# Kernel tuning notes

Measured on AMD Instinct MI355X. Metric: run time of the kernel, lower is better.

## Reference

```python
import jax, jax.numpy as jnp
import numpy as np

DIM, HEADS, RANK = 768, 12, 64
HEAD_DIM = DIM // HEADS

def _xavier(key, shape):
    fan_in, fan_out = shape[1], shape[0]
    std = (2.0 / (fan_in + fan_out)) ** 0.5
    return std * jax.random.normal(key, shape, dtype=jnp.float32)

def setup_inputs() -> dict:
    key = jax.random.key(0)
    ks = jax.random.split(key, 12)
    B, N = 8, 1024
    x = jax.random.normal(ks[0], (B, N, DIM), dtype=jnp.float32)
    params = {}
    for i, nm in enumerate(['Q', 'K', 'V']):
        params[f'W_{nm}0'] = _xavier(ks[1 + 3 * i], (DIM, RANK))
        params[f'W_{nm}1'] = _xavier(ks[2 + 3 * i], (HEADS, RANK))
        params[f'W_{nm}2'] = _xavier(ks[3 + 3 * i], (HEAD_DIM, RANK))
    proj_w = _xavier(ks[10], (DIM, DIM))
    proj_b = jnp.zeros((DIM,), dtype=jnp.float32)
    return dict(x=x, W_Q0=params['W_Q0'], W_Q1=params['W_Q1'], W_Q2=params['W_Q2'],
                W_K0=params['W_K0'], W_K1=params['W_K1'], W_K2=params['W_K2'],
                W_V0=params['W_V0'], W_V1=params['W_V1'], W_V2=params['W_V2'],
                proj_w=proj_w, proj_b=proj_b)

def _cp_proj(xh, W2, W1, W0, B, N, H, hd):
    # xh: [B,N,H,hd]; contract head_dim with W2 and heads with W1 -> [B,N,R], then expand to dim via W0
    t = jnp.einsum('blnd,dr,nr->blr', xh, W2, W1)
    out = jnp.einsum('blr,mr->blm', t, W0)          # [B,N,dim]
    return out.reshape(B, N, H, hd).transpose(0, 2, 1, 3)  # [B,H,N,hd]

def reference(x, W_Q0, W_Q1, W_Q2, W_K0, W_K1, W_K2, W_V0, W_V1, W_V2, proj_w, proj_b):
    B, N, C = x.shape
    H = W_Q1.shape[0]
    hd = C // H
    scale = hd ** -0.5
    xh = x.reshape(B, N, H, hd)
    q = _cp_proj(xh, W_Q2, W_Q1, W_Q0, B, N, H, hd)
    k = _cp_proj(xh, W_K2, W_K1, W_K0, B, N, H, hd)
    v = _cp_proj(xh, W_V2, W_V1, W_V0, B, N, H, hd)
    attn = jax.nn.softmax(jnp.einsum('bhqd,bhkd->bhqk', q, k) * scale, axis=-1)
    out = jnp.einsum('bhqk,bhkd->bhqd', attn, v).transpose(0, 2, 1, 3).reshape(B, N, C)
    return out @ proj_w.T + proj_b
```

## Files before the change

### kernel.cpp

```cpp
#include <hip/hip_runtime.h>

typedef unsigned short u16;
typedef __attribute__((ext_vector_type(8))) short bf16x8;
typedef __attribute__((ext_vector_type(4))) float f32x4;
typedef __attribute__((ext_vector_type(4))) unsigned short u16x4;
typedef __attribute__((ext_vector_type(8))) unsigned short u16x8;

#define AS1 __attribute__((address_space(1)))
#define AS3 __attribute__((address_space(3)))

__device__ __forceinline__ u16 f2b(float f) {
    unsigned u = __float_as_uint(f);
    unsigned r = 0x7fffu + ((u >> 16) & 1u);
    return (u16)((u + r) >> 16);
}

__device__ __forceinline__ unsigned packtrunc(float p0, float p1) {
#if __has_builtin(__builtin_amdgcn_perm)
    return __builtin_amdgcn_perm(__float_as_uint(p1), __float_as_uint(p0), 0x07060302u);
#else
    return (__float_as_uint(p0) >> 16) | (__float_as_uint(p1) & 0xffff0000u);
#endif
}

#if __has_builtin(__builtin_amdgcn_exp2f)
#define EXP2(x) __builtin_amdgcn_exp2f(x)
#else
#define EXP2(x) exp2f(x)
#endif

__device__ unsigned g_cnt[2];
__device__ unsigned g_gen[2];

__device__ __forceinline__ void gbar(int i, unsigned nblk) {
    __syncthreads();
    if (threadIdx.x == 0) {
        __threadfence();
        const unsigned my = __hip_atomic_load(&g_gen[i], __ATOMIC_RELAXED,
                                              __HIP_MEMORY_SCOPE_AGENT);
        const unsigned v = __hip_atomic_fetch_add(&g_cnt[i], 1u, __ATOMIC_ACQ_REL,
                                                  __HIP_MEMORY_SCOPE_AGENT);
        if (v == nblk - 1u) {
            __hip_atomic_store(&g_cnt[i], 0u, __ATOMIC_RELAXED,
                               __HIP_MEMORY_SCOPE_AGENT);
            __threadfence();
            __hip_atomic_fetch_add(&g_gen[i], 1u, __ATOMIC_ACQ_REL,
                                   __HIP_MEMORY_SCOPE_AGENT);
        } else {
            unsigned spins = 0;
            while (__hip_atomic_load(&g_gen[i], __ATOMIC_ACQUIRE,
                                     __HIP_MEMORY_SCOPE_AGENT) == my) {
                __builtin_amdgcn_s_sleep(2);
                if (++spins > (1u << 22)) break;
            }
        }
        __threadfence();
    }
    __syncthreads();
}

__device__ __forceinline__ void phaseA(
    const int bid, const int t, char* smem,
    const float* __restrict__ X,
    const float* __restrict__ Wq0, const float* __restrict__ Wq1, const float* __restrict__ Wq2,
    const float* __restrict__ Wk0, const float* __restrict__ Wk1, const float* __restrict__ Wk2,
    const float* __restrict__ Wv0, const float* __restrict__ Wv1, const float* __restrict__ Wv2,
    const float* __restrict__ PW,
    u16* __restrict__ T, u16* __restrict__ tvt,
    u16* __restrict__ MqkT, u16* __restrict__ Dcat)
{
    const f32x4 zero4 = {0.f, 0.f, 0.f, 0.f};
    if (bid < 384) {
        u16*   As  = (u16*)smem;
        u16*   Bs  = (u16*)(smem + 8192);
        float* W1t = (float*)(smem + 16384);
        float* W2t = (float*)(smem + 19456);

        const int lane = t & 63, wv = t >> 6;
        const int l15 = lane & 15, quad = lane >> 4;

        const int lin = bid;
        const int xcd = lin & 7, j = lin >> 3;
        const int col = j % 3, rowhi = j / 3;
        const int rowBase = (rowhi * 8 + xcd) * 64;
        const int colBase = col * 64;

        const float* W1g = (col == 0) ? Wq1 : (col == 1) ? Wk1 : Wv1;
        const float* W2g = (col == 0) ? Wq2 : (col == 1) ? Wk2 : Wv2;
        for (int i = t; i < 768; i += 256) W1t[i] = W1g[i];
        for (int i = t; i < 4096; i += 256) {
            const int d = i >> 6, r = i & 63;
            W2t[r * 65 + d] = W2g[i];
        }

        const int srow = t >> 2;
        const int sc4  = t & 3;
        const int scol = sc4 * 16;
        const int swa = ((sc4 * 2)     ^ (srow & 7)) * 8;
        const int swb = ((sc4 * 2 + 1) ^ (srow & 7)) * 8;
        const float* aS = X + (size_t)(rowBase + srow) * 768 + scol;

        float4 a0 = *(const float4*)(aS);
        float4 a1 = *(const float4*)(aS + 4);
        float4 a2 = *(const float4*)(aS + 8);
        float4 a3 = *(const float4*)(aS + 12);

        f32x4 acc[4];
#pragma unroll
        for (int tn = 0; tn < 4; ++tn) acc[tn] = zero4;

        for (int kk = 0; kk < 768; kk += 64) {
            __syncthreads();
            u16x8 ap0, ap1;
            ap0[0] = f2b(a0.x); ap0[1] = f2b(a0.y); ap0[2] = f2b(a0.z); ap0[3] = f2b(a0.w);
            ap0[4] = f2b(a1.x); ap0[5] = f2b(a1.y); ap0[6] = f2b(a1.z); ap0[7] = f2b(a1.w);
            ap1[0] = f2b(a2.x); ap1[1] = f2b(a2.y); ap1[2] = f2b(a2.z); ap1[3] = f2b(a2.w);
            ap1[4] = f2b(a3.x); ap1[5] = f2b(a3.y); ap1[6] = f2b(a3.z); ap1[7] = f2b(a3.w);
            *(u16x8*)&As[srow * 64 + swa] = ap0;
            *(u16x8*)&As[srow * 64 + swb] = ap1;
            {
                const int c0 = kk + scol;
                const int hh = c0 >> 6, dd = c0 & 63;
                const float w1v = W1t[hh * 64 + srow];
                u16x8 bp0, bp1;
#pragma unroll
                for (int jj = 0; jj < 8; ++jj)
                    bp0[jj] = f2b(w1v * W2t[srow * 65 + dd + jj]);
#pragma unroll
                for (int jj = 0; jj < 8; ++jj)
                    bp1[jj] = f2b(w1v * W2t[srow * 65 + dd + 8 + jj]);
                *(u16x8*)&Bs[srow * 64 + swa] = bp0;
                *(u16x8*)&Bs[srow * 64 + swb] = bp1;
            }
            __syncthreads();

            if (kk < 704) {
                a0 = *(const float4*)(aS + kk + 64);
                a1 = *(const float4*)(aS + kk + 68);
                a2 = *(const float4*)(aS + kk + 72);
                a3 = *(const float4*)(aS + kk + 76);
            }

            const int arow = wv * 16 + l15;
#pragma unroll
            for (int ks = 0; ks < 2; ++ks) {
                const bf16x8 af = *(const bf16x8*)
                    &As[arow * 64 + ((ks * 4 + quad) ^ (arow & 7)) * 8];
#pragma unroll
                for (int tn = 0; tn < 4; ++tn) {
                    const int brow = tn * 16 + l15;
                    const bf16x8 bf = *(const bf16x8*)
                        &Bs[brow * 64 + ((ks * 4 + quad) ^ (brow & 7)) * 8];
                    acc[tn] = __builtin_amdgcn_mfma_f32_16x16x32_bf16(af, bf, acc[tn], 0, 0, 0);
                }
            }
        }

        if (colBase < 128) {
#pragma unroll
            for (int tn = 0; tn < 4; ++tn) {
                const int c = colBase + tn * 16 + l15;
#pragma unroll
                for (int r = 0; r < 4; ++r) {
                    const int grow = rowBase + wv * 16 + quad * 4 + r;
                    T[(size_t)grow * 128 + c] = f2b(acc[tn][r]);
                }
            }
        } else {
#pragma unroll
            for (int tn = 0; tn < 4; ++tn) {
                const int rr = tn * 16 + l15;
                const int grow = rowBase + wv * 16 + quad * 4;
                u16x4 pk;
                pk.x = f2b(acc[tn][0]); pk.y = f2b(acc[tn][1]);
                pk.z = f2b(acc[tn][2]); pk.w = f2b(acc[tn][3]);
                *(u16x4*)(tvt + (size_t)rr * 8192 + grow) = pk;
            }
        }
    } else if (bid < 432) {
        float* wq = (float*)smem;
        float* wk = (float*)(smem + 16640);
        const int hq = bid - 384;
        const int h = hq >> 2, quarter = hq & 3;
        const float qs = 0.125f * 1.4426950408889634f;
        for (int i = t; i < 4096; i += 256) {
            const int dd = i >> 6, r = i & 63;
            wq[dd * 65 + r] = Wq0[(h * 64 + dd) * 64 + r] * qs;
            wk[dd * 65 + r] = Wk0[(h * 64 + dd) * 64 + r];
        }
        __syncthreads();
        const int j0 = quarter * 1024 + t * 4;
        const int r2 = j0 >> 6, r1b = j0 & 63;
        u16x4 pk;
#pragma unroll
        for (int jj = 0; jj < 4; ++jj) {
            float acc = 0.f;
#pragma unroll
            for (int dd = 0; dd < 64; ++dd)
                acc += wk[dd * 65 + r2] * wq[dd * 65 + r1b + jj];
            ((u16*)&pk)[jj] = f2b(acc);
        }
        *(u16x4*)(MqkT + (size_t)(h * 64 + r2) * 64 + r1b) = pk;
    } else if (bid < 720) {
        float* w0s = (float*)smem;
        float* pws = (float*)(smem + 16640);
        const int hb = bid - 432;
        const int h = hb / 24, mBase = (hb - h * 24) * 32;
        for (int i = t; i < 4096; i += 256) {
            const int d = i >> 6, r = i & 63;
            w0s[d * 65 + r] = Wv0[(h * 64 + d) * 64 + r];
        }
        for (int i = t; i < 2048; i += 256) {
            const int mi = i >> 6, d = i & 63;
            pws[mi * 65 + d] = PW[(size_t)(mBase + mi) * 768 + h * 64 + d];
        }
        __syncthreads();
        const int r = t & 63, mi0 = t >> 6;
        float w0c[64];
#pragma unroll
        for (int d = 0; d < 64; ++d) w0c[d] = w0s[d * 65 + r];
        for (int mi = mi0; mi < 32; mi += 4) {
            float acc = 0.f;
#pragma unroll
            for (int d = 0; d < 64; ++d) acc += pws[mi * 65 + d] * w0c[d];
            Dcat[(size_t)(mBase + mi) * 768 + h * 64 + r] = f2b(acc);
        }
    }
}

__device__ __forceinline__ void phaseB(
    const int bid, const int t, char* smem,
    const u16* __restrict__ T, const u16* __restrict__ MqkT,
    const u16* __restrict__ tvt, u16* __restrict__ Zcat)
{
    const int bh = bid % 96;
    const int qt = bid / 96;
    const int b = bh / 12, h = bh - b * 12;
    const u16* qp = T + ((size_t)b * 1024 + qt * 128) * 128;
    const u16* kp = T + (size_t)b * 1024 * 128 + 64;
    const u16* vp = tvt + b * 1024;

    u16* const B0raw = (u16*)smem;
    u16* const B1raw = (u16*)(smem + 18432);

    const int lane = t & 63, wv = t >> 6;
    const int l15 = lane & 15, quad = lane >> 4;
    const f32x4 zero4 = {0.f, 0.f, 0.f, 0.f};

    bf16x8 qf[2][2];
#pragma unroll
    for (int qg = 0; qg < 2; ++qg) {
        const u16* qrow = qp + (size_t)(wv * 32 + qg * 16 + l15) * 128;
        qf[qg][0] = *(const bf16x8*)(qrow + quad * 8);
        qf[qg][1] = *(const bf16x8*)(qrow + 32 + quad * 8);
    }

    const int srow = t >> 2;
    const int scol = (t & 3) * 16;
    const int p5 = srow & 31;
    const int lrow = (srow & 32) | ((p5 & 4) << 2) | ((p5 & 16) >> 1)
                   | ((p5 & 8) >> 1) | (p5 & 3);

    bf16x8 vone = {};
    if (l15 == 0) {
#pragma unroll
        for (int j = 0; j < 8; ++j) vone[j] = (short)0x3F80;
    }

    int4 kr0 = *(const int4*)(kp + (size_t)srow * 128 + scol);
    int4 kr1 = *(const int4*)(kp + (size_t)srow * 128 + scol + 8);
    int4 vr0 = *(const int4*)(vp + (size_t)srow * 8192 + scol);
    int4 vr1 = *(const int4*)(vp + (size_t)srow * 8192 + scol + 8);

    {
        f32x4 Wt[2][4];
#pragma unroll
        for (int qg = 0; qg < 2; ++qg)
#pragma unroll
            for (int tn = 0; tn < 4; ++tn) Wt[qg][tn] = zero4;
#pragma unroll
        for (int ks = 0; ks < 2; ++ks) {
#pragma unroll
            for (int tn = 0; tn < 4; ++tn) {
                const bf16x8 mb = *(const bf16x8*)(
                    MqkT + (size_t)(h * 64 + tn * 16 + l15) * 64 + ks * 32 + quad * 8);
                Wt[0][tn] = __builtin_amdgcn_mfma_f32_16x16x32_bf16(qf[0][ks], mb, Wt[0][tn], 0, 0, 0);
                Wt[1][tn] = __builtin_amdgcn_mfma_f32_16x16x32_bf16(qf[1][ks], mb, Wt[1][tn], 0, 0, 0);
            }
        }
#pragma unroll
        for (int qg = 0; qg < 2; ++qg)
#pragma unroll
            for (int tn = 0; tn < 4; ++tn)
#pragma unroll
                for (int r = 0; r < 4; ++r)
                    B1raw[(wv * 32 + qg * 16 + quad * 4 + r) * 72 + tn * 16 + l15] =
                        f2b(Wt[qg][tn][r]);
    }
    __syncthreads();
    bf16x8 wf[2][2];
#pragma unroll
    for (int qg = 0; qg < 2; ++qg) {
        wf[qg][0] = *(const bf16x8*)&B1raw[(wv * 32 + qg * 16 + l15) * 72 + quad * 8];
        wf[qg][1] = *(const bf16x8*)&B1raw[(wv * 32 + qg * 16 + l15) * 72 + 32 + quad * 8];
    }

    *(int4*)&B0raw[lrow * 72 + scol]                 = kr0;
    *(int4*)&B0raw[lrow * 72 + scol + 8]             = kr1;
    *(int4*)&B0raw[64 * 72 + srow * 72 + scol]       = vr0;
    *(int4*)&B0raw[64 * 72 + srow * 72 + scol + 8]   = vr1;
    kr0 = *(const int4*)(kp + (size_t)(64 + srow) * 128 + scol);
    kr1 = *(const int4*)(kp + (size_t)(64 + srow) * 128 + scol + 8);
    vr0 = *(const int4*)(vp + (size_t)srow * 8192 + 64 + scol);
    vr1 = *(const int4*)(vp + (size_t)srow * 8192 + 64 + scol + 8);
    __syncthreads();

    f32x4 o_acc[2][4];
    f32x4 Lacc[2] = {zero4, zero4};
#pragma unroll
    for (int qg = 0; qg < 2; ++qg)
#pragma unroll
        for (int tn = 0; tn < 4; ++tn) o_acc[qg][tn] = zero4;

#define STAGE(NB)                                                               \
    {                                                                           \
        *(int4*)&NB[lrow * 72 + scol]               = kr0;                      \
        *(int4*)&NB[lrow * 72 + scol + 8]           = kr1;                      \
        *(int4*)&NB[64 * 72 + srow * 72 + scol]     = vr0;                      \
        *(int4*)&NB[64 * 72 + srow * 72 + scol + 8] = vr1;                      \
    }
#define PREFETCH(KT)                                                            \
    {                                                                           \
        kr0 = *(const int4*)(kp + (size_t)((KT) * 64 + srow) * 128 + scol);     \
        kr1 = *(const int4*)(kp + (size_t)((KT) * 64 + srow) * 128 + scol + 8); \
        vr0 = *(const int4*)(vp + (size_t)srow * 8192 + (KT) * 64 + scol);      \
        vr1 = *(const int4*)(vp + (size_t)srow * 8192 + (KT) * 64 + scol + 8);  \
    }
#define FLASH_TILE(KB)                                                          \
    {                                                                           \
        f32x4 Sacc[2][4];                                                       \
        _Pragma("unroll")                                                       \
        for (int qg = 0; qg < 2; ++qg)                                          \
            _Pragma("unroll")                                                   \
            for (int tk = 0; tk < 4; ++tk) Sacc[qg][tk] = zero4;                \
        _Pragma("unroll")                                                       \
        for (int ks = 0; ks < 2; ++ks) {                                        \
            _Pragma("unroll")                                                   \
            for (int tk = 0; tk < 4; ++tk) {                                    \
                const bf16x8 kf = *(const bf16x8*)&KB[(tk * 16 + l15) * 72 + ks * 32 + quad * 8]; \
                Sacc[0][tk] = __builtin_amdgcn_mfma_f32_16x16x32_bf16(kf, wf[0][ks], Sacc[0][tk], 0, 0, 0); \
                Sacc[1][tk] = __builtin_amdgcn_mfma_f32_16x16x32_bf16(kf, wf[1][ks], Sacc[1][tk], 0, 0, 0); \
            }                                                                   \
        }                                                                       \
        union { bf16x8 v; unsigned u[4]; } pf[2][2];                            \
        _Pragma("unroll")                                                       \
        for (int qg = 0; qg < 2; ++qg)                                          \
            _Pragma("unroll")                                                   \
            for (int tk = 0; tk < 4; ++tk) {                                    \
                const float p0 = EXP2(Sacc[qg][tk][0]);                         \
                const float p1 = EXP2(Sacc[qg][tk][1]);                         \
                const float p2 = EXP2(Sacc[qg][tk][2]);                         \
                const float p3 = EXP2(Sacc[qg][tk][3]);                         \
                const int g = tk >> 1, hf = (tk & 1) * 2;                       \
                pf[qg][g].u[hf + 0] = packtrunc(p0, p1);                        \
                pf[qg][g].u[hf + 1] = packtrunc(p2, p3);                        \
            }                                                                   \
        _Pragma("unroll")                                                       \
        for (int g = 0; g < 2; ++g) {                                           \
            _Pragma("unroll")                                                   \
            for (int tn = 0; tn < 4; ++tn) {                                    \
                const bf16x8 vf = *(const bf16x8*)&KB[64 * 72 + (tn * 16 + l15) * 72 + g * 32 + quad * 8]; \
                o_acc[0][tn] = __builtin_amdgcn_mfma_f32_16x16x32_bf16(pf[0][g].v, vf, o_acc[0][tn], 0, 0, 0); \
                o_acc[1][tn] = __builtin_amdgcn_mfma_f32_16x16x32_bf16(pf[1][g].v, vf, o_acc[1][tn], 0, 0, 0); \
            }                                                                   \
            Lacc[0] = __builtin_amdgcn_mfma_f32_16x16x32_bf16(pf[0][g].v, vone, Lacc[0], 0, 0, 0); \
            Lacc[1] = __builtin_amdgcn_mfma_f32_16x16x32_bf16(pf[1][g].v, vone, Lacc[1], 0, 0, 0); \
        }                                                                       \
    }

    for (int t8 = 0; t8 < 8; ++t8) {
        const int kt0 = 2 * t8;
        STAGE(B1raw);
        if (t8 < 7) PREFETCH(kt0 + 2);
        FLASH_TILE(B0raw);
        __syncthreads();
        if (t8 < 7) {
            STAGE(B0raw);
            PREFETCH(kt0 + 3);
        }
        FLASH_TILE(B1raw);
        if (t8 < 7) __syncthreads();
    }

#undef STAGE
#undef PREFETCH
#undef FLASH_TILE

#pragma unroll
    for (int qg = 0; qg < 2; ++qg) {
#pragma unroll
        for (int r = 0; r < 4; ++r) {
            const float Lv = __shfl(Lacc[qg][r], quad << 4, 64);
            const float inv = 1.0f / Lv;
            const int token = qt * 128 + wv * 32 + qg * 16 + quad * 4 + r;
#pragma unroll
            for (int tn = 0; tn < 4; ++tn) {
                const int col = h * 64 + tn * 16 + l15;
                Zcat[(size_t)(b * 1024 + token) * 768 + col] = f2b(o_acc[qg][tn][r] * inv);
            }
        }
    }
}

__device__ __forceinline__ void phaseC(
    const int bid, const int t, char* smem,
    const u16* __restrict__ Zcat, const u16* __restrict__ Dcat,
    float* __restrict__ outp, const float* __restrict__ bias)
{
    u16* As = (u16*)smem;
    u16* Bs = (u16*)(smem + 16384);

    const int lane = t & 63, wv = t >> 6;
    const int l15 = lane & 15, quad = lane >> 4;
    const f32x4 zero4 = {0.f, 0.f, 0.f, 0.f};

    const int lin = bid;
    const int xcd = lin & 7, j = lin >> 3;
    const int colT = j % 12, rowhi = j / 12;
    const int rowBase = (rowhi * 8 + xcd) * 128;
    const int colBase = colT * 64;

    const int srowA = wv * 32 + (lane >> 2);
    const int srowB = wv * 16 + (lane >> 2);
    const int sc4   = lane & 3;
    const int scol  = sc4 * 16;
    const int swa0 = ((sc4 * 2)     ^ (srowA & 7)) * 8;
    const int swa1 = ((sc4 * 2 + 1) ^ (srowA & 7)) * 8;
    const int swb0 = ((sc4 * 2)     ^ (srowB & 7)) * 8;
    const int swb1 = ((sc4 * 2 + 1) ^ (srowB & 7)) * 8;
    const u16* aSrc = Zcat + (size_t)(rowBase + srowA) * 768 + scol;
    const u16* bSrc = Dcat + (size_t)(colBase + srowB) * 768 + scol;

    int4 ar0 = *(const int4*)(aSrc);
    int4 ar1 = *(const int4*)(aSrc + 8);
    int4 ar2 = *(const int4*)(aSrc + 16 * 768);
    int4 ar3 = *(const int4*)(aSrc + 16 * 768 + 8);
    int4 br0 = *(const int4*)(bSrc);
    int4 br1 = *(const int4*)(bSrc + 8);

    f32x4 acc[2][4];
#pragma unroll
    for (int tm = 0; tm < 2; ++tm)
#pragma unroll
        for (int tn = 0; tn < 4; ++tn) acc[tm][tn] = zero4;

    for (int kk = 0; kk < 768; kk += 64) {
        __syncthreads();
        *(int4*)&As[srowA * 64 + swa0]        = ar0;
        *(int4*)&As[srowA * 64 + swa1]        = ar1;
        *(int4*)&As[(srowA + 16) * 64 + swa0] = ar2;
        *(int4*)&As[(srowA + 16) * 64 + swa1] = ar3;
        *(int4*)&Bs[srowB * 64 + swb0]        = br0;
        *(int4*)&Bs[srowB * 64 + swb1]        = br1;
        __syncthreads();

        if (kk < 704) {
            ar0 = *(const int4*)(aSrc + kk + 64);
            ar1 = *(const int4*)(aSrc + kk + 72);
            ar2 = *(const int4*)(aSrc + 16 * 768 + kk + 64);
            ar3 = *(const int4*)(aSrc + 16 * 768 + kk + 72);
            br0 = *(const int4*)(bSrc + kk + 64);
            br1 = *(const int4*)(bSrc + kk + 72);
        }

#pragma unroll
        for (int ks = 0; ks < 2; ++ks) {
            bf16x8 af[2], bfm[4];
#pragma unroll
            for (int tm = 0; tm < 2; ++tm) {
                const int arow = wv * 32 + tm * 16 + l15;
                af[tm] = *(const bf16x8*)
                    &As[arow * 64 + ((ks * 4 + quad) ^ (arow & 7)) * 8];
            }
#pragma unroll
            for (int tn = 0; tn < 4; ++tn) {
                const int brow = tn * 16 + l15;
                bfm[tn] = *(const bf16x8*)
                    &Bs[brow * 64 + ((ks * 4 + quad) ^ (brow & 7)) * 8];
            }
#pragma unroll
            for (int tm = 0; tm < 2; ++tm)
#pragma unroll
                for (int tn = 0; tn < 4; ++tn)
                    acc[tm][tn] = __builtin_amdgcn_mfma_f32_16x16x32_bf16(
                        af[tm], bfm[tn], acc[tm][tn], 0, 0, 0);
        }
    }

#pragma unroll
    for (int tm = 0; tm < 2; ++tm) {
        const int grow = rowBase + wv * 32 + tm * 16 + quad * 4;
#pragma unroll
        for (int tn = 0; tn < 4; ++tn) {
            const int gcol = colBase + tn * 16 + l15;
            const float bv = bias[gcol];
#pragma unroll
            for (int r = 0; r < 4; ++r)
                outp[(size_t)(grow + r) * 768 + gcol] = acc[tm][tn][r] + bv;
        }
    }
}

__global__ __launch_bounds__(256, 3) void mega(
    const float* __restrict__ X,
    const float* __restrict__ Wq0, const float* __restrict__ Wq1, const float* __restrict__ Wq2,
    const float* __restrict__ Wk0, const float* __restrict__ Wk1, const float* __restrict__ Wk2,
    const float* __restrict__ Wv0, const float* __restrict__ Wv1, const float* __restrict__ Wv2,
    const float* __restrict__ PW, const float* __restrict__ bias,
    u16* __restrict__ T, u16* __restrict__ tvt,
    u16* __restrict__ MqkT, u16* __restrict__ Dcat,
    u16* __restrict__ Zcat, float* __restrict__ outp)
{
    __shared__ __align__(16) char smem[36864];
    const int bid = blockIdx.x, t = threadIdx.x;
    if (bid < 720)
        phaseA(bid, t, smem, X, Wq0, Wq1, Wq2, Wk0, Wk1, Wk2, Wv0, Wv1, Wv2, PW,
               T, tvt, MqkT, Dcat);
    gbar(0, 768u);
    phaseB(bid, t, smem, T, MqkT, tvt, Zcat);
    gbar(1, 768u);
    phaseC(bid, t, smem, Zcat, Dcat, outp, bias);
}

__global__ __launch_bounds__(256, 2) void k_prep(
    const float* __restrict__ X,
    const float* __restrict__ Wq0, const float* __restrict__ Wq1, const float* __restrict__ Wq2,
    const float* __restrict__ Wk0, const float* __restrict__ Wk1, const float* __restrict__ Wk2,
    const float* __restrict__ Wv0, const float* __restrict__ Wv1, const float* __restrict__ Wv2,
    const float* __restrict__ PW,
    u16* __restrict__ T, u16* __restrict__ tvt,
    u16* __restrict__ MqkT, u16* __restrict__ Dcat)
{
    __shared__ __align__(16) char smem[36864];
    phaseA(blockIdx.x, threadIdx.x, smem, X, Wq0, Wq1, Wq2, Wk0, Wk1, Wk2,
           Wv0, Wv1, Wv2, PW, T, tvt, MqkT, Dcat);
}

__global__ __launch_bounds__(256, 3) void k_flash(
    const u16* __restrict__ T, const u16* __restrict__ MqkT,
    const u16* __restrict__ tvt, u16* __restrict__ Zcat)
{
    __shared__ __align__(16) char smem[36864];
    phaseB(blockIdx.x + 96 * blockIdx.y, threadIdx.x, smem, T, MqkT, tvt, Zcat);
}

__global__ __launch_bounds__(256, 3) void k_out(
    const u16* __restrict__ Zcat, const u16* __restrict__ Dcat,
    float* __restrict__ outp, const float* __restrict__ bias)
{
    __shared__ __align__(16) char smem[36864];
    phaseC(blockIdx.x, threadIdx.x, smem, Zcat, Dcat, outp, bias);
}

extern "C" void kernel_launch(void* const* d_in, const int* in_sizes, int n_in,
                              void* d_out, int out_size, void* d_ws, size_t ws_size,
                              hipStream_t stream)
{
    const float* x      = (const float*)d_in[0];
    const float* Wq0    = (const float*)d_in[1];
    const float* Wq1    = (const float*)d_in[2];
    const float* Wq2    = (const float*)d_in[3];
    const float* Wk0    = (const float*)d_in[4];
    const float* Wk1    = (const float*)d_in[5];
    const float* Wk2    = (const float*)d_in[6];
    const float* Wv0    = (const float*)d_in[7];
    const float* Wv1    = (const float*)d_in[8];
    const float* Wv2    = (const float*)d_in[9];
    const float* proj_w = (const float*)d_in[10];
    const float* proj_b = (const float*)d_in[11];
    float* outp = (float*)d_out;

    char* ws = (char*)d_ws;
    u16* T    = (u16*)ws;
    u16* tvt  = (u16*)(ws + 2097152);
    u16* MqkT = (u16*)(ws + 3440640);
    u16* Dcat = (u16*)(ws + 3538944);
    u16* Zcat = (u16*)(ws + 4718592);

    static int use_mega = -1;
    if (use_mega < 0) {
        int nb = 0;
        hipError_t e = hipOccupancyMaxActiveBlocksPerMultiprocessor(&nb, mega, 256, 0);
        use_mega = (e == hipSuccess && nb >= 3) ? 1 : 0;
    }

    if (use_mega) {
        mega<<<768, 256, 0, stream>>>(x, Wq0, Wq1, Wq2, Wk0, Wk1, Wk2,
                                      Wv0, Wv1, Wv2, proj_w, proj_b,
                                      T, tvt, MqkT, Dcat, Zcat, outp);
    } else {
        k_prep<<<720, 256, 0, stream>>>(x, Wq0, Wq1, Wq2, Wk0, Wk1, Wk2,
                                        Wv0, Wv1, Wv2, proj_w,
                                        T, tvt, MqkT, Dcat);
        k_flash<<<dim3(96, 8), 256, 0, stream>>>(T, MqkT, tvt, Zcat);
        k_out<<<768, 256, 0, stream>>>(Zcat, Dcat, outp, proj_b);
    }
}
```

Measured before the change: 155.2 us.

## Spread phase-A projection GEMM over all 768 blocks with 32-row tiles

Phase A's low-rank projection GEMM moves from 384 blocks with 64-row tiles to all 768 blocks with 32-row tiles. Each wave now computes a 16x32 sub-tile instead of 16x64. The MqkT and Dcat precompute tasks are stacked onto the first 336 blocks after the GEMM, with an extra barrier to reuse shared memory. The goal is to use the whole grid in phase A and shorten its critical path before the global barrier, at the cost of building the B operand twice as often per output row and unbalanced work on the first blocks.

Measured after the change: 167.9 us. 8.2% more time.

```diff
diff --git a/kernel.cpp b/kernel.cpp
--- a/kernel.cpp
+++ b/kernel.cpp
@@ -70,11 +70,11 @@
     u16* __restrict__ MqkT, u16* __restrict__ Dcat)
 {
     const f32x4 zero4 = {0.f, 0.f, 0.f, 0.f};
-    if (bid < 384) {
+    {
         u16*   As  = (u16*)smem;
-        u16*   Bs  = (u16*)(smem + 8192);
-        float* W1t = (float*)(smem + 16384);
-        float* W2t = (float*)(smem + 19456);
+        u16*   Bs  = (u16*)(smem + 4096);
+        float* W1t = (float*)(smem + 12288);
+        float* W2t = (float*)(smem + 15360);
 
         const int lane = t & 63, wv = t >> 6;
         const int l15 = lane & 15, quad = lane >> 4;
@@ -82,7 +82,7 @@
         const int lin = bid;
         const int xcd = lin & 7, j = lin >> 3;
         const int col = j % 3, rowhi = j / 3;
-        const int rowBase = (rowhi * 8 + xcd) * 64;
+        const int rowBase = (rowhi * 8 + xcd) * 32;
         const int colBase = col * 64;
 
         const float* W1g = (col == 0) ? Wq1 : (col == 1) ? Wk1 : Wv1;
@@ -93,33 +93,35 @@
             W2t[r * 65 + d] = W2g[i];
         }
 
+        const int arow_s = t >> 3;
+        const int ach    = t & 7;
+        const int aswz   = (ach ^ (arow_s & 7)) * 8;
+        const float* aS  = X + (size_t)(rowBase + arow_s) * 768 + ach * 8;
+
         const int srow = t >> 2;
         const int sc4  = t & 3;
-        const int scol = sc4 * 16;
+        const int scolB = sc4 * 16;
         const int swa = ((sc4 * 2)     ^ (srow & 7)) * 8;
         const int swb = ((sc4 * 2 + 1) ^ (srow & 7)) * 8;
-        const float* aS = X + (size_t)(rowBase + srow) * 768 + scol;
 
         float4 a0 = *(const float4*)(aS);
         float4 a1 = *(const float4*)(aS + 4);
-        float4 a2 = *(const float4*)(aS + 8);
-        float4 a3 = *(const float4*)(aS + 12);
-
-        f32x4 acc[4];
-#pragma unroll
-        for (int tn = 0; tn < 4; ++tn) acc[tn] = zero4;
+
+        f32x4 acc[2];
+        acc[0] = zero4; acc[1] = zero4;
+
+        const int rG = wv & 1;
+        const int cG = wv >> 1;
+        const int arow = rG * 16 + l15;
 
         for (int kk = 0; kk < 768; kk += 64) {
             __syncthreads();
-            u16x8 ap0, ap1;
-            ap0[0] = f2b(a0.x); ap0[1] = f2b(a0.y); ap0[2] = f2b(a0.z); ap0[3] = f2b(a0.w);
-            ap0[4] = f2b(a1.x); ap0[5] = f2b(a1.y); ap0[6] = f2b(a1.z); ap0[7] = f2b(a1.w);
-            ap1[0] = f2b(a2.x); ap1[1] = f2b(a2.y); ap1[2] = f2b(a2.z); ap1[3] = f2b(a2.w);
-            ap1[4] = f2b(a3.x); ap1[5] = f2b(a3.y); ap1[6] = f2b(a3.z); ap1[7] = f2b(a3.w);
-            *(u16x8*)&As[srow * 64 + swa] = ap0;
-            *(u16x8*)&As[srow * 64 + swb] = ap1;
+            u16x8 ap;
+            ap[0] = f2b(a0.x); ap[1] = f2b(a0.y); ap[2] = f2b(a0.z); ap[3] = f2b(a0.w);
+            ap[4] = f2b(a1.x); ap[5] = f2b(a1.y); ap[6] = f2b(a1.z); ap[7] = f2b(a1.w);
+            *(u16x8*)&As[arow_s * 64 + aswz] = ap;
             {
-                const int c0 = kk + scol;
+                const int c0 = kk + scolB;
                 const int hh = c0 >> 6, dd = c0 & 63;
                 const float w1v = W1t[hh * 64 + srow];
                 u16x8 bp0, bp1;
@@ -137,50 +139,50 @@
             if (kk < 704) {
                 a0 = *(const float4*)(aS + kk + 64);
                 a1 = *(const float4*)(aS + kk + 68);
-                a2 = *(const float4*)(aS + kk + 72);
-                a3 = *(const float4*)(aS + kk + 76);
-            }
-
-            const int arow = wv * 16 + l15;
+            }
+
 #pragma unroll
             for (int ks = 0; ks < 2; ++ks) {
                 const bf16x8 af = *(const bf16x8*)
                     &As[arow * 64 + ((ks * 4 + quad) ^ (arow & 7)) * 8];
 #pragma unroll
-                for (int tn = 0; tn < 4; ++tn) {
-                    const int brow = tn * 16 + l15;
+                for (int tnl = 0; tnl < 2; ++tnl) {
+                    const int brow = (cG * 2 + tnl) * 16 + l15;
                     const bf16x8 bf = *(const bf16x8*)
                         &Bs[brow * 64 + ((ks * 4 + quad) ^ (brow & 7)) * 8];
-                    acc[tn] = __builtin_amdgcn_mfma_f32_16x16x32_bf16(af, bf, acc[tn], 0, 0, 0);
+                    acc[tnl] = __builtin_amdgcn_mfma_f32_16x16x32_bf16(af, bf, acc[tnl], 0, 0, 0);
                 }
             }
         }
 
         if (colBase < 128) {
 #pragma unroll
-            for (int tn = 0; tn < 4; ++tn) {
-                const int c = colBase + tn * 16 + l15;
+            for (int tnl = 0; tnl < 2; ++tnl) {
+                const int c = colBase + (cG * 2 + tnl) * 16 + l15;
 #pragma unroll
                 for (int r = 0; r < 4; ++r) {
-                    const int grow = rowBase + wv * 16 + quad * 4 + r;
-                    T[(size_t)grow * 128 + c] = f2b(acc[tn][r]);
+                    const int grow = rowBase + rG * 16 + quad * 4 + r;
+                    T[(size_t)grow * 128 + c] = f2b(acc[tnl][r]);
                 }
             }
         } else {
 #pragma unroll
-            for (int tn = 0; tn < 4; ++tn) {
-                const int rr = tn * 16 + l15;
-                const int grow = rowBase + wv * 16 + quad * 4;
+            for (int tnl = 0; tnl < 2; ++tnl) {
+                const int rr = (cG * 2 + tnl) * 16 + l15;
+                const int grow = rowBase + rG * 16 + quad * 4;
                 u16x4 pk;
-                pk.x = f2b(acc[tn][0]); pk.y = f2b(acc[tn][1]);
-                pk.z = f2b(acc[tn][2]); pk.w = f2b(acc[tn][3]);
+                pk.x = f2b(acc[tnl][0]); pk.y = f2b(acc[tnl][1]);
+                pk.z = f2b(acc[tnl][2]); pk.w = f2b(acc[tnl][3]);
                 *(u16x4*)(tvt + (size_t)rr * 8192 + grow) = pk;
             }
         }
-    } else if (bid < 432) {
+    }
+
+    if (bid < 48) {
+        __syncthreads();
         float* wq = (float*)smem;
         float* wk = (float*)(smem + 16640);
-        const int hq = bid - 384;
+        const int hq = bid;
         const int h = hq >> 2, quarter = hq & 3;
         const float qs = 0.125f * 1.4426950408889634f;
         for (int i = t; i < 4096; i += 256) {
@@ -201,10 +203,11 @@
             ((u16*)&pk)[jj] = f2b(acc);
         }
         *(u16x4*)(MqkT + (size_t)(h * 64 + r2) * 64 + r1b) = pk;
-    } else if (bid < 720) {
+    } else if (bid < 336) {
+        __syncthreads();
         float* w0s = (float*)smem;
         float* pws = (float*)(smem + 16640);
-        const int hb = bid - 432;
+        const int hb = bid - 48;
         const int h = hb / 24, mBase = (hb - h * 24) * 32;
         for (int i = t; i < 4096; i += 256) {
             const int d = i >> 6, r = i & 63;
@@ -523,9 +526,8 @@
 {
     __shared__ __align__(16) char smem[36864];
     const int bid = blockIdx.x, t = threadIdx.x;
-    if (bid < 720)
-        phaseA(bid, t, smem, X, Wq0, Wq1, Wq2, Wk0, Wk1, Wk2, Wv0, Wv1, Wv2, PW,
-               T, tvt, MqkT, Dcat);
+    phaseA(bid, t, smem, X, Wq0, Wq1, Wq2, Wk0, Wk1, Wk2, Wv0, Wv1, Wv2, PW,
+           T, tvt, MqkT, Dcat);
     gbar(0, 768u);
     phaseB(bid, t, smem, T, MqkT, tvt, Zcat);
     gbar(1, 768u);
@@ -599,7 +601,7 @@
                                       Wv0, Wv1, Wv2, proj_w, proj_b,
                                       T, tvt, MqkT, Dcat, Zcat, outp);
     } else {
-        k_prep<<<720, 256, 0, stream>>>(x, Wq0, Wq1, Wq2, Wk0, Wk1, Wk2,
+        k_prep<<<768, 256, 0, stream>>>(x, Wq0, Wq1, Wq2, Wk0, Wk1, Wk2,
                                         Wv0, Wv1, Wv2, proj_w,
                                         T, tvt, MqkT, Dcat);
         k_flash<<<dim3(96, 8), 256, 0, stream>>>(T, MqkT, tvt, Zcat);
```

## Replace first global barrier with per-batch dataflow counters

Applied to the files above, without the earlier changes.

Removes the grid-wide barrier between phase A and phase B. Producer blocks now bump per-batch and Mqk completion counters, and each phase-B block waits only for the T/tvt rows of its own batch plus the Mqk blocks, using a generation-based target taken from g_gen[1]. This lets attention blocks start while other batches are still projecting, cutting barrier skew, at the cost of spin polling and some fragility in the counter bookkeeping across launches. phaseA is now called for all block ids, which relies on it handling bid >= 720 safely.

New measurement: 175.2 us. +12.9%, slower.

```diff
diff --git a/kernel.cpp b/kernel.cpp
--- a/kernel.cpp
+++ b/kernel.cpp
@@ -31,6 +31,8 @@
 
 __device__ unsigned g_cnt[2];
 __device__ unsigned g_gen[2];
+__device__ unsigned g_acnt[8];
+__device__ unsigned g_mcnt;
 
 __device__ __forceinline__ void gbar(int i, unsigned nblk) {
     __syncthreads();
@@ -177,6 +179,12 @@
                 *(u16x4*)(tvt + (size_t)rr * 8192 + grow) = pk;
             }
         }
+        __syncthreads();
+        if (t == 0) {
+            __threadfence();
+            __hip_atomic_fetch_add(&g_acnt[rowBase >> 10], 1u, __ATOMIC_RELEASE,
+                                   __HIP_MEMORY_SCOPE_AGENT);
+        }
     } else if (bid < 432) {
         float* wq = (float*)smem;
         float* wk = (float*)(smem + 16640);
@@ -201,6 +209,12 @@
             ((u16*)&pk)[jj] = f2b(acc);
         }
         *(u16x4*)(MqkT + (size_t)(h * 64 + r2) * 64 + r1b) = pk;
+        __syncthreads();
+        if (t == 0) {
+            __threadfence();
+            __hip_atomic_fetch_add(&g_mcnt, 1u, __ATOMIC_RELEASE,
+                                   __HIP_MEMORY_SCOPE_AGENT);
+        }
     } else if (bid < 720) {
         float* w0s = (float*)smem;
         float* pws = (float*)(smem + 16640);
@@ -523,10 +537,31 @@
 {
     __shared__ __align__(16) char smem[36864];
     const int bid = blockIdx.x, t = threadIdx.x;
-    if (bid < 720)
-        phaseA(bid, t, smem, X, Wq0, Wq1, Wq2, Wk0, Wk1, Wk2, Wv0, Wv1, Wv2, PW,
-               T, tvt, MqkT, Dcat);
-    gbar(0, 768u);
+
+    const unsigned G = __hip_atomic_load(&g_gen[1], __ATOMIC_ACQUIRE,
+                                         __HIP_MEMORY_SCOPE_AGENT);
+
+    phaseA(bid, t, smem, X, Wq0, Wq1, Wq2, Wk0, Wk1, Wk2, Wv0, Wv1, Wv2, PW,
+           T, tvt, MqkT, Dcat);
+
+    {
+        const int b_need = (bid % 96) / 12;
+        __syncthreads();
+        if (t == 0) {
+            const unsigned tgt = 48u * (G + 1u);
+            unsigned spins = 0;
+            while (__hip_atomic_load(&g_acnt[b_need], __ATOMIC_ACQUIRE,
+                                     __HIP_MEMORY_SCOPE_AGENT) < tgt ||
+                   __hip_atomic_load(&g_mcnt, __ATOMIC_ACQUIRE,
+                                     __HIP_MEMORY_SCOPE_AGENT) < tgt) {
+                __builtin_amdgcn_s_sleep(2);
+                if (++spins > (1u << 22)) break;
+            }
+            __threadfence();
+        }
+        __syncthreads();
+    }
+
     phaseB(bid, t, smem, T, MqkT, tvt, Zcat);
     gbar(1, 768u);
     phaseC(bid, t, smem, Zcat, Dcat, outp, bias);
```
